# Kernel tuning notes

Measured on AMD Instinct MI355X. Metric: run time of the kernel, lower is better.

The kernel has to match this reference:

```python
import jax, jax.numpy as jnp
import numpy as np
from jax import lax

N_HEADS = 12
HEAD_DIM = 64
ALPHA = 4.0  # spikingjelly surrogate.Sigmoid default alpha
EPS = 1e-5   # BatchNorm1d default eps

@jax.custom_vjp
def _heaviside(v):
    return (v >= 0.0).astype(v.dtype)

def _heaviside_fwd(v):
    return _heaviside(v), v

def _heaviside_bwd(v, g):
    sg = jax.nn.sigmoid(ALPHA * v)
    return (g * ALPHA * sg * (1.0 - sg),)

_heaviside.defvjp(_heaviside_fwd, _heaviside_bwd)

def if_node(x):
    """Multi-step IFNode (v_threshold=1, hard reset to 0), scan over leading T dim."""
    def step(v, xt):
        v = v + xt                      # integrate
        s = _heaviside(v - 1.0)         # fire
        v = (1.0 - s) * v               # hard reset: spiked neurons -> 0
        return v, s
    _, spikes = lax.scan(step, jnp.zeros_like(x[0]), x)
    return spikes

def bn1d(x):
    """Fresh (training-mode) BatchNorm1d over (T, S, D) with channels=S;
    affine weight=1, bias=0 at init, so pure normalization over axes (0,2)."""
    mean = x.mean(axis=(0, 2), keepdims=True)
    var = x.var(axis=(0, 2), keepdims=True)  # biased variance, as torch BN uses
    return (x - mean) * lax.rsqrt(var + EPS)

def setup_inputs() -> dict:
    key = jax.random.key(0)
    ks = jax.random.split(key, 5)
    T, S, D = 4, 2048, 768
    x = jax.random.normal(ks[0], (T, S, D), dtype=jnp.float32)
    scale = 0.02
    wq = jax.random.normal(ks[1], (D, D), dtype=jnp.float32) * scale
    wk = jax.random.normal(ks[2], (D, D), dtype=jnp.float32) * scale
    wv = jax.random.normal(ks[3], (D, D), dtype=jnp.float32) * scale
    wo = jax.random.normal(ks[4], (D, D), dtype=jnp.float32) * scale
    return {"x": x, "wq": wq, "wk": wk, "wv": wv, "wo": wo, "cur_pos": S}

def reference(x, wq, wk, wv, wo, cur_pos):
    T, S, D = x.shape
    tmp = if_node(x)                    # init_spike
    Q = tmp @ wq
    V = tmp @ wv
    K = tmp @ wk
    Q = if_node(bn1d(Q))                # spike_q(bnq(Q))
    V = if_node(bn1d(V))                # spike_v(bnv(V))
    K = if_node(bn1d(K))                # spike_k(bnk(K))
    # (T, S, H, hd) -> (T, H, S, hd)
    Qh = Q.reshape(T, S, N_HEADS, HEAD_DIM).transpose(0, 2, 1, 3)
    Vh = V.reshape(T, S, N_HEADS, HEAD_DIM).transpose(0, 2, 1, 3)
    Kh = K.reshape(T, S, N_HEADS, HEAD_DIM).transpose(0, 2, 1, 3)
    QK = (Qh * Kh).sum(axis=2, keepdims=True)   # (T, H, 1, hd)
    QK = if_node(QK)                    # talking_heads
    QKV = Vh * QK                       # (T, H, S, hd)
    QKV = QKV.transpose(0, 2, 1, 3).reshape(T, S, D)
    return bn1d(QKV @ wo)
```

## Files before the change

kernel.cpp:

```cpp
#include <hip/hip_runtime.h>

#define T_ 4
#define S_ 2048
#define D_ 768
#define SD_ (S_ * D_)
#define TSD_ (T_ * SD_)
#define H_ 12
#define HD_ 64
#define PLANE_BYTES 2359296u

typedef int int32x4 __attribute__((ext_vector_type(4)));

__device__ __forceinline__ void cp16(unsigned char* lds, const unsigned char* g) {
    __builtin_amdgcn_global_load_lds(
        (const __attribute__((address_space(1))) unsigned int*)g,
        (__attribute__((address_space(3))) unsigned int*)lds, 16, 0, 0);
}

__device__ __forceinline__ size_t frag_addr(int m, int d) {
    return ((size_t)(m >> 4) * 12 + (d >> 6)) * 1024 +
           (size_t)(((d >> 4) & 3) * 256 + (m & 15) * 16 + (d & 15));
}

__global__ __launch_bounds__(256) void k_prep_all(const float* __restrict__ wq,
                                                  const float* __restrict__ wk,
                                                  const float* __restrict__ wv,
                                                  const float* __restrict__ wo,
                                                  const float* __restrict__ x,
                                                  unsigned char* __restrict__ Bp,
                                                  unsigned char* __restrict__ Sx,
                                                  unsigned int* __restrict__ QKp) {
    __shared__ unsigned char wl[4096];
    int tid = threadIdx.x;
    if (blockIdx.y < 4) {
        const float* W = (blockIdx.y == 0) ? wq : (blockIdx.y == 1) ? wk
                       : (blockIdx.y == 2) ? wv : wo;
        unsigned char* out = Bp + (size_t)blockIdx.y * PLANE_BYTES;
        int c = blockIdx.x;
        int kb = c % 12;
        int nbg = c / 12;
        int k_loc = tid >> 2;
        int n_base = (tid & 3) * 4;
        float4 w4 = *(const float4*)(
            W + (size_t)(kb * 64 + k_loc) * D_ + nbg * 16 + n_base);
        float wsv[4] = {w4.x, w4.y, w4.z, w4.w};
#pragma unroll
        for (int j = 0; j < 4; j++) {
            int n_loc = n_base + j;
            int u = (int)rintf(wsv[j] * 1073741824.0f);
#pragma unroll
            for (int p = 0; p < 4; p++) {
                wl[p * 1024 + (n_loc + 16 * (k_loc >> 4)) * 16 + (k_loc & 15)] =
                    (unsigned char)(u & 255);
                u = (u + 128) >> 8;
            }
        }
        __syncthreads();
        int p = tid >> 6;
        int lane = tid & 63;
        uint4 val = *(const uint4*)&wl[p * 1024 + lane * 16];
        *(uint4*)(out + (size_t)((p * 48 + nbg) * 12 + kb) * 1024 + lane * 16) =
            val;
    } else {
        if (blockIdx.x >= 384) {
            if (blockIdx.x < 432) {
                int idx = (blockIdx.x - 384) * 256 + tid;
                QKp[idx] = 0u;
            }
            return;
        }
        int gid = blockIdx.x * 256 + tid;
        int s = gid / 48;
        int d0 = (gid % 48) * 16;
        double v[16];
#pragma unroll
        for (int j = 0; j < 16; j++) v[j] = 0.0;
#pragma unroll
        for (int t = 0; t < T_; t++) {
            union { uint4 u; unsigned char b[16]; } sp;
#pragma unroll
            for (int q = 0; q < 4; q++) {
                float4 xt = *(const float4*)(
                    x + (size_t)t * SD_ + (size_t)s * D_ + d0 + q * 4);
                float xs[4] = {xt.x, xt.y, xt.z, xt.w};
#pragma unroll
                for (int j = 0; j < 4; j++) {
                    int jj = q * 4 + j;
                    v[jj] += (double)xs[j];
                    unsigned char ss = (v[jj] >= 1.0) ? 1 : 0;
                    sp.b[jj] = ss;
                    if (ss) v[jj] = 0.0;
                }
            }
            *(uint4*)(Sx + frag_addr(t * S_ + s, d0)) = sp.u;
        }
    }
}

__global__ __launch_bounds__(256, 2) void k_gemm_i8(
    const unsigned char* __restrict__ A,
    const unsigned char* __restrict__ Bp,
    const unsigned int* __restrict__ Mp,
    float* __restrict__ C0, float* __restrict__ C1, float* __restrict__ C2,
    int bzoff) {
    int z = blockIdx.z;
    const unsigned char* B = Bp + (size_t)(bzoff + z) * PLANE_BYTES;
    float* C = (z == 0) ? C0 : (z == 1) ? C1 : C2;

    __shared__ __align__(16) unsigned char bsm[2 * 32768];
    __shared__ __align__(16) unsigned int maskw[192];

    int tid = threadIdx.x;
    int lane = tid & 63;
    int w = tid >> 6;
    int wm = w >> 1;
    int wn = w & 1;
    int row0 = blockIdx.x * 128;
    int tI = row0 >> 11;
    int n0 = blockIdx.y * 64;
    int nbg0 = blockIdx.y * 4;
    int col = lane & 15;
    int quad = lane >> 4;

    int32x4 zerov = {0, 0, 0, 0};
    int32x4 acc[4][2][4];
#pragma unroll
    for (int mb = 0; mb < 4; mb++)
#pragma unroll
        for (int nb = 0; nb < 2; nb++)
#pragma unroll
            for (int p = 0; p < 4; p++) acc[mb][nb][p] = zerov;

    const unsigned char* Ab =
        A + (size_t)((row0 >> 4) + wm * 4) * 12 * 1024 + lane * 16;

    auto stageB = [&](int buf, int kb2) {
        unsigned char* bb = bsm + buf * 32768;
#pragma unroll
        for (int kk = 0; kk < 2; kk++)
#pragma unroll
            for (int qi = 0; qi < 4; qi++) {
                int q = w * 4 + qi;
                int p = q >> 2, nb = q & 3;
                cp16(bb + kk * 16384 + q * 1024,
                     B + (size_t)((p * 48 + nbg0 + nb) * 12 + 2 * kb2 + kk) *
                             1024 + lane * 16);
            }
    };

    stageB(0, 0);
    if (Mp && tid < 192) {
        unsigned int m = 0;
#pragma unroll
        for (int c = 0; c < 16; c++) m |= Mp[c * 768 + tI * 192 + tid];
        maskw[tid] = m;
    }
    int32x4 a[2][4];
#pragma unroll
    for (int mb = 0; mb < 4; mb++)
        a[0][mb] = *(const int32x4*)(Ab + (size_t)(mb * 12) * 1024);
    __syncthreads();

    for (int kb2 = 0; kb2 < 6; kb2++) {
        int cur = kb2 & 1;
        if (kb2 < 5) stageB(1 - cur, kb2 + 1);
#pragma unroll
        for (int kbh = 0; kbh < 2; kbh++) {
            int kb = kb2 * 2 + kbh;
            if (kb < 11) {
#pragma unroll
                for (int mb = 0; mb < 4; mb++)
                    a[(kb + 1) & 1][mb] = *(const int32x4*)(
                        Ab + (size_t)(mb * 12 + kb + 1) * 1024);
            }
            int32x4 af[4];
#pragma unroll
            for (int mb = 0; mb < 4; mb++) af[mb] = a[kb & 1][mb];
            if (Mp) {
                int32x4 mv = *(const int32x4*)(
                    (const unsigned char*)maskw + kb * 64 + quad * 16);
#pragma unroll
                for (int mb = 0; mb < 4; mb++) af[mb] &= mv;
            }
            const unsigned char* bb = bsm + cur * 32768 + kbh * 16384;
#pragma unroll
            for (int p = 0; p < 4; p++)
#pragma unroll
                for (int nb = 0; nb < 2; nb++) {
                    int32x4 bf = *(const int32x4*)(
                        bb + (size_t)(p * 4 + wn * 2 + nb) * 1024 + lane * 16);
#pragma unroll
                    for (int mb = 0; mb < 4; mb++)
                        acc[mb][nb][p] = __builtin_amdgcn_mfma_i32_16x16x64_i8(
                            af[mb], bf, acc[mb][nb][p], 0, 0, 0);
                }
        }
        __syncthreads();
    }

#pragma unroll
    for (int mb = 0; mb < 4; mb++)
#pragma unroll
        for (int nb = 0; nb < 2; nb++)
#pragma unroll
            for (int r = 0; r < 4; r++) {
                double td = (double)acc[mb][nb][0][r]
                          + 256.0 * (double)acc[mb][nb][1][r]
                          + 65536.0 * (double)acc[mb][nb][2][r]
                          + 16777216.0 * (double)acc[mb][nb][3][r];
                float v = (float)(td * (1.0 / 1073741824.0));
                int rr = row0 + wm * 64 + mb * 16 + quad * 4 + r;
                int cc = n0 + wn * 32 + nb * 16 + col;
                C[(size_t)rr * D_ + cc] = v;
            }
}

__global__ __launch_bounds__(256) void k_bnif_qk(const float* __restrict__ Qf,
                                                 const float* __restrict__ Kf,
                                                 const float* __restrict__ Vf,
                                                 unsigned char* __restrict__ Vs,
                                                 unsigned int* __restrict__ QKp) {
    int s = blockIdx.x;
    __shared__ float buf[3][T_][D_];
    __shared__ double red[8];
    __shared__ unsigned char spkV[T_ * D_];
    __shared__ unsigned char spkA[T_ * D_];
    __shared__ double stats[3][2];

    int tid = threadIdx.x;
    const float* Xs[3] = {Qf, Kf, Vf};
#pragma unroll
    for (int y = 0; y < 3; y++) {
        double sum = 0.0, sumsq = 0.0;
#pragma unroll
        for (int t = 0; t < T_; t++) {
            for (int d = tid; d < D_; d += 256) {
                float v = Xs[y][(size_t)t * SD_ + (size_t)s * D_ + d];
                buf[y][t][d] = v;
                double dv = (double)v;
                sum += dv;
                sumsq += dv * dv;
            }
        }
#pragma unroll
        for (int off = 32; off > 0; off >>= 1) {
            sum += __shfl_down(sum, off);
            sumsq += __shfl_down(sumsq, off);
        }
        int lane = tid & 63, wv = tid >> 6;
        if (lane == 0) { red[wv] = sum; red[4 + wv] = sumsq; }
        __syncthreads();
        if (tid == 0) {
            double s4 = red[0] + red[1] + red[2] + red[3];
            double q4 = red[4] + red[5] + red[6] + red[7];
            double mean = s4 / 3072.0;
            double var = q4 / 3072.0 - mean * mean;
            stats[y][0] = mean;
            stats[y][1] = 1.0 / sqrt(var + 1e-5);
        }
        __syncthreads();
    }

    for (int d = tid; d < D_; d += 256) {
        unsigned char qs[T_], ks[T_];
#pragma unroll
        for (int y = 0; y < 3; y++) {
            double mean = stats[y][0], rstd = stats[y][1];
            double v = 0.0;
#pragma unroll
            for (int t = 0; t < T_; t++) {
                double xn = ((double)buf[y][t][d] - mean) * rstd;
                v += xn;
                unsigned char sp = (v >= 1.0) ? 1 : 0;
                if (y == 0) qs[t] = sp;
                else if (y == 1) ks[t] = sp;
                else spkV[t * D_ + d] = sp;
                if (sp) v = 0.0;
            }
        }
#pragma unroll
        for (int t = 0; t < T_; t++) spkA[t * D_ + d] = qs[t] & ks[t];
    }
    __syncthreads();

    if (tid < 192) {
        int tt = tid / 48, gg = tid % 48;
        uint4 val = *(const uint4*)&spkV[tt * D_ + gg * 16];
        size_t dst = ((size_t)(tt * 128 + (s >> 4)) * 12 + (gg >> 2)) * 1024 +
                     (size_t)((gg & 3) * 256 + (s & 15) * 16);
        *(uint4*)(Vs + dst) = val;
        unsigned int* dstq = QKp + (s & 15) * 768;
#pragma unroll
        for (int t = 0; t < T_; t++) {
            unsigned int word = *(const unsigned int*)&spkA[t * D_ + tid * 4];
            if (word) atomicOr(dstq + t * 192 + tid, word);
        }
    }
}

__global__ __launch_bounds__(256) void k_bn_out(const float* __restrict__ Xin,
                                                float* __restrict__ out) {
    int s = blockIdx.x;
    __shared__ float buf[T_][D_];
    __shared__ double red[16];
    int tid = threadIdx.x;
    double sum = 0.0, sumsq = 0.0;
#pragma unroll
    for (int t = 0; t < T_; t++) {
        for (int d = tid; d < D_; d += 256) {
            float v = Xin[(size_t)t * SD_ + (size_t)s * D_ + d];
            buf[t][d] = v;
            double dv = (double)v;
            sum += dv;
            sumsq += dv * dv;
        }
    }
#pragma unroll
    for (int off = 32; off > 0; off >>= 1) {
        sum += __shfl_down(sum, off);
        sumsq += __shfl_down(sumsq, off);
    }
    int lane = tid & 63, wv = tid >> 6;
    if (lane == 0) { red[wv] = sum; red[4 + wv] = sumsq; }
    __syncthreads();
    if (tid == 0) {
        double s4 = red[0] + red[1] + red[2] + red[3];
        double q4 = red[4] + red[5] + red[6] + red[7];
        double mean = s4 / 3072.0;
        double var = q4 / 3072.0 - mean * mean;
        red[8] = mean;
        red[9] = 1.0 / sqrt(var + 1e-5);
    }
    __syncthreads();
    double mean = red[8], rstd = red[9];
    for (int d = tid; d < D_; d += 256) {
#pragma unroll
        for (int t = 0; t < T_; t++) {
            double v = (double)buf[t][d];
            out[(size_t)t * SD_ + (size_t)s * D_ + d] =
                (float)((v - mean) * rstd);
        }
    }
}

extern "C" void kernel_launch(void* const* d_in, const int* in_sizes, int n_in,
                              void* d_out, int out_size, void* d_ws,
                              size_t ws_size, hipStream_t stream) {
    const float* x  = (const float*)d_in[0];
    const float* wq = (const float*)d_in[1];
    const float* wk = (const float*)d_in[2];
    const float* wv = (const float*)d_in[3];
    const float* wo = (const float*)d_in[4];
    float* out = (float*)d_out;

    float* ws  = (float*)d_ws;
    float* Qf  = ws;
    float* Kf  = ws + (size_t)TSD_;
    float* Vf  = ws + (size_t)2 * TSD_;
    unsigned int* QKp = (unsigned int*)(ws + (size_t)3 * TSD_);
    unsigned char* Sx = (unsigned char*)(QKp + 12288);
    unsigned char* Vs = Sx + (size_t)TSD_;
    unsigned char* Bp = Vs + (size_t)TSD_;

    k_prep_all<<<dim3(576, 5), 256, 0, stream>>>(wq, wk, wv, wo, x, Bp, Sx,
                                                 QKp);
    k_gemm_i8<<<dim3(64, 12, 3), 256, 0, stream>>>(Sx, Bp, nullptr,
                                                   Qf, Kf, Vf, 0);
    k_bnif_qk<<<S_, 256, 0, stream>>>(Qf, Kf, Vf, Vs, QKp);
    k_gemm_i8<<<dim3(64, 12, 1), 256, 0, stream>>>(Vs, Bp, QKp, Qf, Qf, Qf, 3);
    k_bn_out<<<S_, 256, 0, stream>>>(Qf, out);
}
```

Before: 227.1 us.

## Stage A via LDS in int8 GEMM pipeline; vectorize BN reduction kernels

Measured after the change: 230.6 us. Within noise of the previous version (+1.5%).

```diff
diff --git a/kernel.cpp b/kernel.cpp
--- a/kernel.cpp
+++ b/kernel.cpp
@@ -97,6 +97,8 @@
     }
 }
 
+#define GBUF 24576
+
 __global__ __launch_bounds__(256, 2) void k_gemm_i8(
     const unsigned char* __restrict__ A,
     const unsigned char* __restrict__ Bp,
@@ -107,7 +109,7 @@
     const unsigned char* B = Bp + (size_t)(bzoff + z) * PLANE_BYTES;
     float* C = (z == 0) ? C0 : (z == 1) ? C1 : C2;
 
-    __shared__ __align__(16) unsigned char bsm[2 * 32768];
+    __shared__ __align__(16) unsigned char lds[2 * GBUF];
     __shared__ __align__(16) unsigned int maskw[192];
 
     int tid = threadIdx.x;
@@ -122,6 +124,26 @@
     int col = lane & 15;
     int quad = lane >> 4;
 
+    const unsigned char* Ag = A + (size_t)(row0 >> 4) * 12 * 1024 + lane * 16;
+    const unsigned char* Bg = B + lane * 16;
+
+    auto stage = [&](int buf, int kb) {
+        unsigned char* dst = lds + buf * GBUF;
+#pragma unroll
+        for (int i = 0; i < 2; i++) {
+            int mc = w * 2 + i;
+            cp16(dst + mc * 1024, Ag + (size_t)(mc * 12 + kb) * 1024);
+        }
+#pragma unroll
+        for (int qi = 0; qi < 4; qi++) {
+            int q = w * 4 + qi;
+            int p = q >> 2;
+            int nb = q & 3;
+            cp16(dst + 8192 + q * 1024,
+                 Bg + (size_t)((p * 48 + nbg0 + nb) * 12 + kb) * 1024);
+        }
+    };
+
     int32x4 zerov = {0, 0, 0, 0};
     int32x4 acc[4][2][4];
 #pragma unroll
@@ -131,72 +153,63 @@
 #pragma unroll
             for (int p = 0; p < 4; p++) acc[mb][nb][p] = zerov;
 
-    const unsigned char* Ab =
-        A + (size_t)((row0 >> 4) + wm * 4) * 12 * 1024 + lane * 16;
-
-    auto stageB = [&](int buf, int kb2) {
-        unsigned char* bb = bsm + buf * 32768;
-#pragma unroll
-        for (int kk = 0; kk < 2; kk++)
-#pragma unroll
-            for (int qi = 0; qi < 4; qi++) {
-                int q = w * 4 + qi;
-                int p = q >> 2, nb = q & 3;
-                cp16(bb + kk * 16384 + q * 1024,
-                     B + (size_t)((p * 48 + nbg0 + nb) * 12 + 2 * kb2 + kk) *
-                             1024 + lane * 16);
-            }
-    };
-
-    stageB(0, 0);
+    stage(0, 0);
+    stage(1, 1);
     if (Mp && tid < 192) {
         unsigned int m = 0;
 #pragma unroll
         for (int c = 0; c < 16; c++) m |= Mp[c * 768 + tI * 192 + tid];
         maskw[tid] = m;
     }
-    int32x4 a[2][4];
-#pragma unroll
-    for (int mb = 0; mb < 4; mb++)
-        a[0][mb] = *(const int32x4*)(Ab + (size_t)(mb * 12) * 1024);
-    __syncthreads();
-
-    for (int kb2 = 0; kb2 < 6; kb2++) {
-        int cur = kb2 & 1;
-        if (kb2 < 5) stageB(1 - cur, kb2 + 1);
-#pragma unroll
-        for (int kbh = 0; kbh < 2; kbh++) {
-            int kb = kb2 * 2 + kbh;
-            if (kb < 11) {
+    asm volatile("s_waitcnt vmcnt(0)" ::: "memory");
+    __syncthreads();
+
+    auto kstep = [&](int kb, int cur, bool dostage, bool last) {
+        if (last) asm volatile("s_waitcnt vmcnt(0)" ::: "memory");
+        else      asm volatile("s_waitcnt vmcnt(6)" ::: "memory");
+        __builtin_amdgcn_sched_barrier(0);
+        __builtin_amdgcn_s_barrier();
+        asm volatile("" ::: "memory");
+        __builtin_amdgcn_sched_barrier(0);
+        const unsigned char* Ab = lds + cur * GBUF;
+        const unsigned char* Bb = Ab + 8192;
+        __builtin_amdgcn_s_setprio(1);
+        int32x4 af[4];
+#pragma unroll
+        for (int mb = 0; mb < 4; mb++)
+            af[mb] = *(const int32x4*)(Ab + (wm * 4 + mb) * 1024 + lane * 16);
+        if (Mp) {
+            int32x4 mv = *(const int32x4*)((const unsigned char*)maskw +
+                                           kb * 64 + quad * 16);
+#pragma unroll
+            for (int mb = 0; mb < 4; mb++) af[mb] &= mv;
+        }
+#pragma unroll
+        for (int p = 0; p < 4; p++)
+#pragma unroll
+            for (int nb = 0; nb < 2; nb++) {
+                int32x4 bf = *(const int32x4*)(
+                    Bb + (p * 4 + wn * 2 + nb) * 1024 + lane * 16);
 #pragma unroll
                 for (int mb = 0; mb < 4; mb++)
-                    a[(kb + 1) & 1][mb] = *(const int32x4*)(
-                        Ab + (size_t)(mb * 12 + kb + 1) * 1024);
-            }
-            int32x4 af[4];
-#pragma unroll
-            for (int mb = 0; mb < 4; mb++) af[mb] = a[kb & 1][mb];
-            if (Mp) {
-                int32x4 mv = *(const int32x4*)(
-                    (const unsigned char*)maskw + kb * 64 + quad * 16);
-#pragma unroll
-                for (int mb = 0; mb < 4; mb++) af[mb] &= mv;
-            }
-            const unsigned char* bb = bsm + cur * 32768 + kbh * 16384;
-#pragma unroll
-            for (int p = 0; p < 4; p++)
-#pragma unroll
-                for (int nb = 0; nb < 2; nb++) {
-                    int32x4 bf = *(const int32x4*)(
-                        bb + (size_t)(p * 4 + wn * 2 + nb) * 1024 + lane * 16);
-#pragma unroll
-                    for (int mb = 0; mb < 4; mb++)
-                        acc[mb][nb][p] = __builtin_amdgcn_mfma_i32_16x16x64_i8(
-                            af[mb], bf, acc[mb][nb][p], 0, 0, 0);
-                }
-        }
-        __syncthreads();
-    }
+                    acc[mb][nb][p] = __builtin_amdgcn_mfma_i32_16x16x64_i8(
+                        af[mb], bf, acc[mb][nb][p], 0, 0, 0);
+            }
+        __builtin_amdgcn_s_setprio(0);
+        asm volatile("s_waitcnt lgkmcnt(0)" ::: "memory");
+        __builtin_amdgcn_sched_barrier(0);
+        __builtin_amdgcn_s_barrier();
+        asm volatile("" ::: "memory");
+        __builtin_amdgcn_sched_barrier(0);
+        if (dostage) stage(cur, kb + 2);
+    };
+
+    for (int kb2 = 0; kb2 < 5; kb2++) {
+        kstep(2 * kb2, 0, true, false);
+        kstep(2 * kb2 + 1, 1, true, false);
+    }
+    kstep(10, 0, false, false);
+    kstep(11, 1, false, true);
 
 #pragma unroll
     for (int mb = 0; mb < 4; mb++)
@@ -222,44 +235,57 @@
                                                  unsigned int* __restrict__ QKp) {
     int s = blockIdx.x;
     __shared__ float buf[3][T_][D_];
-    __shared__ double red[8];
+    __shared__ double red[4][6];
     __shared__ unsigned char spkV[T_ * D_];
     __shared__ unsigned char spkA[T_ * D_];
     __shared__ double stats[3][2];
 
     int tid = threadIdx.x;
+    int lane = tid & 63, wv = tid >> 6;
     const float* Xs[3] = {Qf, Kf, Vf};
+    double sum[3] = {0.0, 0.0, 0.0}, sumsq[3] = {0.0, 0.0, 0.0};
 #pragma unroll
     for (int y = 0; y < 3; y++) {
-        double sum = 0.0, sumsq = 0.0;
-#pragma unroll
-        for (int t = 0; t < T_; t++) {
-            for (int d = tid; d < D_; d += 256) {
-                float v = Xs[y][(size_t)t * SD_ + (size_t)s * D_ + d];
-                buf[y][t][d] = v;
-                double dv = (double)v;
-                sum += dv;
-                sumsq += dv * dv;
-            }
-        }
-#pragma unroll
-        for (int off = 32; off > 0; off >>= 1) {
-            sum += __shfl_down(sum, off);
-            sumsq += __shfl_down(sumsq, off);
-        }
-        int lane = tid & 63, wv = tid >> 6;
-        if (lane == 0) { red[wv] = sum; red[4 + wv] = sumsq; }
-        __syncthreads();
-        if (tid == 0) {
-            double s4 = red[0] + red[1] + red[2] + red[3];
-            double q4 = red[4] + red[5] + red[6] + red[7];
-            double mean = s4 / 3072.0;
-            double var = q4 / 3072.0 - mean * mean;
-            stats[y][0] = mean;
-            stats[y][1] = 1.0 / sqrt(var + 1e-5);
-        }
-        __syncthreads();
-    }
+#pragma unroll
+        for (int i = 0; i < 3; i++) {
+            int idx = i * 256 + tid;
+            int t = idx / 192;
+            int c = idx - t * 192;
+            float4 v = *(const float4*)(
+                Xs[y] + (size_t)t * SD_ + (size_t)s * D_ + c * 4);
+            *(float4*)&buf[y][t][c * 4] = v;
+            sum[y] += ((double)v.x + (double)v.y) +
+                      ((double)v.z + (double)v.w);
+            sumsq[y] += ((double)v.x * v.x + (double)v.y * v.y) +
+                        ((double)v.z * v.z + (double)v.w * v.w);
+        }
+    }
+#pragma unroll
+    for (int off = 32; off > 0; off >>= 1) {
+#pragma unroll
+        for (int y = 0; y < 3; y++) {
+            sum[y] += __shfl_down(sum[y], off);
+            sumsq[y] += __shfl_down(sumsq[y], off);
+        }
+    }
+    if (lane == 0) {
+#pragma unroll
+        for (int y = 0; y < 3; y++) {
+            red[wv][y] = sum[y];
+            red[wv][3 + y] = sumsq[y];
+        }
+    }
+    __syncthreads();
+    if (tid < 3) {
+        double s4 = red[0][tid] + red[1][tid] + red[2][tid] + red[3][tid];
+        double q4 = red[0][3 + tid] + red[1][3 + tid] + red[2][3 + tid] +
+                    red[3][3 + tid];
+        double mean = s4 / 3072.0;
+        double var = q4 / 3072.0 - mean * mean;
+        stats[tid][0] = mean;
+        stats[tid][1] = 1.0 / sqrt(var + 1e-5);
+    }
+    __syncthreads();
 
     for (int d = tid; d < D_; d += 256) {
         unsigned char qs[T_], ks[T_];
@@ -301,45 +327,50 @@
 __global__ __launch_bounds__(256) void k_bn_out(const float* __restrict__ Xin,
                                                 float* __restrict__ out) {
     int s = blockIdx.x;
-    __shared__ float buf[T_][D_];
-    __shared__ double red[16];
+    __shared__ double red[4][2];
+    __shared__ double st[2];
     int tid = threadIdx.x;
+    int lane = tid & 63, wv = tid >> 6;
+    float4 vv[3];
     double sum = 0.0, sumsq = 0.0;
 #pragma unroll
-    for (int t = 0; t < T_; t++) {
-        for (int d = tid; d < D_; d += 256) {
-            float v = Xin[(size_t)t * SD_ + (size_t)s * D_ + d];
-            buf[t][d] = v;
-            double dv = (double)v;
-            sum += dv;
-            sumsq += dv * dv;
-        }
+    for (int i = 0; i < 3; i++) {
+        int idx = i * 256 + tid;
+        int t = idx / 192, c = idx - t * 192;
+        float4 v = *(const float4*)(
+            Xin + (size_t)t * SD_ + (size_t)s * D_ + c * 4);
+        vv[i] = v;
+        sum += ((double)v.x + (double)v.y) + ((double)v.z + (double)v.w);
+        sumsq += ((double)v.x * v.x + (double)v.y * v.y) +
+                 ((double)v.z * v.z + (double)v.w * v.w);
     }
 #pragma unroll
     for (int off = 32; off > 0; off >>= 1) {
         sum += __shfl_down(sum, off);
         sumsq += __shfl_down(sumsq, off);
     }
-    int lane = tid & 63, wv = tid >> 6;
-    if (lane == 0) { red[wv] = sum; red[4 + wv] = sumsq; }
+    if (lane == 0) { red[wv][0] = sum; red[wv][1] = sumsq; }
     __syncthreads();
     if (tid == 0) {
-        double s4 = red[0] + red[1] + red[2] + red[3];
-        double q4 = red[4] + red[5] + red[6] + red[7];
+        double s4 = red[0][0] + red[1][0] + red[2][0] + red[3][0];
+        double q4 = red[0][1] + red[1][1] + red[2][1] + red[3][1];
         double mean = s4 / 3072.0;
         double var = q4 / 3072.0 - mean * mean;
-        red[8] = mean;
-        red[9] = 1.0 / sqrt(var + 1e-5);
-    }
-    __syncthreads();
-    double mean = red[8], rstd = red[9];
-    for (int d = tid; d < D_; d += 256) {
-#pragma unroll
-        for (int t = 0; t < T_; t++) {
-            double v = (double)buf[t][d];
-            out[(size_t)t * SD_ + (size_t)s * D_ + d] =
-                (float)((v - mean) * rstd);
-        }
+        st[0] = mean;
+        st[1] = 1.0 / sqrt(var + 1e-5);
+    }
+    __syncthreads();
+    double mean = st[0], rstd = st[1];
+#pragma unroll
+    for (int i = 0; i < 3; i++) {
+        int idx = i * 256 + tid;
+        int t = idx / 192, c = idx - t * 192;
+        float4 o;
+        o.x = (float)(((double)vv[i].x - mean) * rstd);
+        o.y = (float)(((double)vv[i].y - mean) * rstd);
+        o.z = (float)(((double)vv[i].z - mean) * rstd);
+        o.w = (float)(((double)vv[i].w - mean) * rstd);
+        *(float4*)(out + (size_t)t * SD_ + (size_t)s * D_ + c * 4) = o;
     }
 }
 
```
